# Kernel tuning notes

Measured on AMD Instinct MI355X. Metric: run time of the kernel, lower is better.

## Reference

```python
import jax, jax.numpy as jnp
import numpy as np

EPS = 1e-5


def setup_inputs() -> dict:
    key = jax.random.key(0)
    ks = jax.random.split(key, 8)
    g, p, d, h, w = 32, 64, 512, 24, 8
    hw = h * w
    return {
        "gal_fea": jax.random.normal(ks[0], (g, d, h, w), dtype=jnp.float32),
        "prob_fea": jax.random.normal(ks[1], (p, d, h, w), dtype=jnp.float32),
        "bn_weight": jnp.ones((1,), jnp.float32),
        "bn_bias": jnp.zeros((1,), jnp.float32),
        "bn_mean": jax.random.normal(ks[2], (1,), jnp.float32) * 0.1,
        "bn_var": jax.random.uniform(ks[3], (1,), jnp.float32, 0.5, 1.5),
        "fc_weight": jax.random.normal(ks[4], (1, 2 * hw), jnp.float32) * 0.05,
        "fc_bias": jnp.zeros((1,), jnp.float32),
        "lbn_weight": jnp.ones((1,), jnp.float32),
        "lbn_bias": jnp.zeros((1,), jnp.float32),
        "lbn_mean": jax.random.normal(ks[5], (1,), jnp.float32) * 0.1,
        "lbn_var": jax.random.uniform(ks[6], (1,), jnp.float32, 0.5, 1.5),
    }


def reference(gal_fea, prob_fea, bn_weight, bn_bias, bn_mean, bn_var,
              fc_weight, fc_bias, lbn_weight, lbn_bias, lbn_mean, lbn_var):
    g, d, h, w = gal_fea.shape
    p = prob_fea.shape[0]
    hw = h * w
    # 1x1 conv with probe pixels as kernels == batched correlation (QK^T style)
    gal = gal_fea.reshape(g, d, hw)                                  # [g, d, hw_x]
    ker = jnp.transpose(prob_fea, (0, 2, 3, 1)).reshape(p, hw, d)    # [p, hw_y, d]
    s = jnp.einsum('gdx,pyd->gpyx', gal, ker)                        # [g, p, hw_y, hw_x]
    # dual-axis max pooling, then concat: [g, p, 2*hw]
    score = jnp.concatenate([s.max(axis=2), s.max(axis=3)], axis=-1)
    # BatchNorm1d(1) in eval mode: scalar affine with running stats
    score = (score - bn_mean) * (bn_weight / jnp.sqrt(bn_var + EPS)) + bn_bias
    # fc: Linear(2*hw, 1)
    score = score.reshape(g * p, 2 * hw) @ fc_weight[0] + fc_bias[0]  # [g*p]
    score = score.reshape(g, p)
    # logit BatchNorm1d(1), eval mode
    score = (score - lbn_mean) * (lbn_weight / jnp.sqrt(lbn_var + EPS)) + lbn_bias
    return jax.nn.sigmoid(score / 10.0)
```

## Files before the change

kernel.cpp:

```cpp
#include <hip/hip_runtime.h>
#include <hip/hip_bf16.h>
#include <cstdint>
#include <cstddef>

#define NG 32
#define NP 64
#define ND 512
#define HW 192
#define EPSV 1e-5f

typedef _Float16 half8 __attribute__((ext_vector_type(8)));
typedef float floatx4 __attribute__((ext_vector_type(4)));
typedef float floatx16 __attribute__((ext_vector_type(16)));

__global__ __launch_bounds__(256) void transpose_cvt_all(const float* __restrict__ gal,
                                                         const float* __restrict__ prob,
                                                         _Float16* __restrict__ galT,
                                                         _Float16* __restrict__ probT) {
  __shared__ float tile[32][33];
  const int z = blockIdx.z;
  const float* sp;
  _Float16* dp;
  if (z < NP) {
    sp = prob + (size_t)z * ND * HW;
    dp = probT + (size_t)z * HW * ND;
  } else {
    sp = gal + (size_t)(z - NP) * ND * HW;
    dp = galT + (size_t)(z - NP) * HW * ND;
  }
  const int k0 = blockIdx.x * 32;
  const int s0 = blockIdx.y * 32;
  const int tx = threadIdx.x & 31, ty = threadIdx.x >> 5;
#pragma unroll
  for (int i = ty; i < 32; i += 8)
    tile[i][tx] = sp[(size_t)(k0 + i) * HW + s0 + tx];
  __syncthreads();
#pragma unroll
  for (int i = ty; i < 32; i += 8)
    dp[(size_t)(s0 + i) * ND + k0 + tx] = (_Float16)tile[tx][i];
}

__device__ __forceinline__ void g2l16(const void* g, void* l) {
  __builtin_amdgcn_global_load_lds(
      (const __attribute__((address_space(1))) void*)g,
      (__attribute__((address_space(3))) void*)l, 16, 0, 0);
}

__global__ __launch_bounds__(256, 2) void qaconv_main(
    const _Float16* __restrict__ galT, const _Float16* __restrict__ probT,
    const float* __restrict__ bn_w, const float* __restrict__ bn_b,
    const float* __restrict__ bn_m, const float* __restrict__ bn_v,
    const float* __restrict__ fc_w, const float* __restrict__ fc_b,
    const float* __restrict__ lbn_w, const float* __restrict__ lbn_b,
    const float* __restrict__ lbn_m, const float* __restrict__ lbn_v,
    float* __restrict__ out) {
  __shared__ __align__(16) char shraw[192 * 66 * 4];
  __shared__ float colpart[2][HW];
  __shared__ float wsum[4];
  char* tileA = shraw;
  char* tileB = shraw + 24576;
  float(*rowbuf)[66] = (float(*)[66])shraw;

  const int bid = blockIdx.x;
  const int g = bid >> 6, p = bid & 63;
  const int t = threadIdx.x;
  const int lane = t & 63, wid = t >> 6;
  const int wr = wid & 1;
  const int wc = wid >> 1;
  const int l31 = lane & 31, hi = lane >> 5;

  const _Float16* pA = probT + (size_t)p * HW * ND;
  const _Float16* pB = galT + (size_t)g * HW * ND;

  floatx16 acc[3][3];
#pragma unroll
  for (int i = 0; i < 3; ++i)
#pragma unroll
    for (int j = 0; j < 3; ++j) acc[i][j] = (floatx16)0.f;

  const int srow = t >> 3;
  const int s = (t & 7) ^ (srow & 7);
  const _Float16* gA = pA + (size_t)srow * ND + s * 8;
  const _Float16* gB = pB + (size_t)srow * ND + s * 8;
  const int ldst = wid * 1024;

  for (int kt = 0; kt < 8; ++kt) {
    const int kb = kt * 64;
    __syncthreads();
#pragma unroll
    for (int r = 0; r < 6; ++r) {
      g2l16(gA + (size_t)r * 32 * ND + kb, tileA + r * 4096 + ldst);
      g2l16(gB + (size_t)r * 32 * ND + kb, tileB + r * 4096 + ldst);
    }
    __syncthreads();
#pragma unroll
    for (int kc = 0; kc < 4; ++kc) {
      half8 af[3], bf[3];
      const int sl = kc * 2 + hi;
#pragma unroll
      for (int f = 0; f < 3; ++f) {
        const int ra = wr * 96 + f * 32 + l31;
        af[f] = *(const half8*)(tileA + ra * 128 + ((sl ^ (ra & 7)) << 4));
        const int rb = wc * 96 + f * 32 + l31;
        bf[f] = *(const half8*)(tileB + rb * 128 + ((sl ^ (rb & 7)) << 4));
      }
      __builtin_amdgcn_s_setprio(1);
#pragma unroll
      for (int i = 0; i < 3; ++i)
#pragma unroll
        for (int j = 0; j < 3; ++j)
          acc[i][j] =
              __builtin_amdgcn_mfma_f32_32x32x16_f16(af[i], bf[j], acc[i][j], 0, 0, 0);
      __builtin_amdgcn_s_setprio(0);
    }
  }

  float cm[3];
#pragma unroll
  for (int fb = 0; fb < 3; ++fb) {
    float v = -3.4e38f;
#pragma unroll
    for (int fa = 0; fa < 3; ++fa)
#pragma unroll
      for (int e = 0; e < 16; ++e) v = fmaxf(v, acc[fa][fb][e]);
    v = fmaxf(v, __shfl_xor(v, 32));
    cm[fb] = v;
  }
  if (lane < 32) {
#pragma unroll
    for (int fb = 0; fb < 3; ++fb) colpart[wr][wc * 96 + fb * 32 + lane] = cm[fb];
  }

  __syncthreads();
#pragma unroll
  for (int fa = 0; fa < 3; ++fa)
#pragma unroll
    for (int e = 0; e < 16; ++e) {
      const float rv =
          fmaxf(fmaxf(acc[fa][0][e], acc[fa][1][e]), acc[fa][2][e]);
      const int Y = wr * 96 + fa * 32 + (e & 3) + 8 * (e >> 2) + 4 * hi;
      rowbuf[Y][wc * 32 + l31] = rv;
    }
  __syncthreads();

  float partial = 0.f;
  if (t < HW) {
    float rmax = -3.4e38f;
#pragma unroll
    for (int j = 0; j < 16; ++j) {
      const floatx4 v = *(const floatx4*)&rowbuf[t][j * 4];
      rmax = fmaxf(rmax, fmaxf(fmaxf(v[0], v[1]), fmaxf(v[2], v[3])));
    }
    const float cmax = fmaxf(colpart[0][t], colpart[1][t]);
    const float scale = bn_w[0] / sqrtf(bn_v[0] + EPSV);
    const float m = bn_m[0], b = bn_b[0];
    partial = ((cmax - m) * scale + b) * fc_w[t] +
              ((rmax - m) * scale + b) * fc_w[HW + t];
  }
#pragma unroll
  for (int off = 1; off < 64; off <<= 1) partial += __shfl_xor(partial, off);
  if (lane == 0) wsum[wid] = partial;
  __syncthreads();
  if (t == 0) {
    const float sum = fc_b[0] + wsum[0] + wsum[1] + wsum[2] + wsum[3];
    const float logit = (sum - lbn_m[0]) * (lbn_w[0] / sqrtf(lbn_v[0] + EPSV)) + lbn_b[0];
    out[bid] = 1.f / (1.f + expf(-logit * 0.1f));
  }
}

__global__ __launch_bounds__(256) void qaconv_naive(
    const float* __restrict__ gal, const float* __restrict__ prob,
    const float* __restrict__ bn_w, const float* __restrict__ bn_b,
    const float* __restrict__ bn_m, const float* __restrict__ bn_v,
    const float* __restrict__ fc_w, const float* __restrict__ fc_b,
    const float* __restrict__ lbn_w, const float* __restrict__ lbn_b,
    const float* __restrict__ lbn_m, const float* __restrict__ lbn_v,
    float* __restrict__ out) {
  __shared__ float prow[ND];
  __shared__ float rowmaxs[HW];
  __shared__ float colmaxs[HW];
  __shared__ float red[4];
  const int bid = blockIdx.x;
  const int g = bid >> 6, p = bid & 63;
  const int t = threadIdx.x, lane = t & 63, wid = t >> 6;
  const float* gp = gal + (size_t)g * ND * HW;
  const float* pp = prob + (size_t)p * ND * HW;
  float colmax = -3.4e38f;
  for (int y = 0; y < HW; ++y) {
    for (int k = t; k < ND; k += 256) prow[k] = pp[(size_t)k * HW + y];
    __syncthreads();
    float sv = -3.4e38f;
    if (t < HW) {
      sv = 0.f;
      for (int k = 0; k < ND; ++k) sv = fmaf(prow[k], gp[(size_t)k * HW + t], sv);
      colmax = fmaxf(colmax, sv);
    }
    float m = sv;
#pragma unroll
    for (int off = 1; off < 64; off <<= 1) m = fmaxf(m, __shfl_xor(m, off));
    if (lane == 0) red[wid] = m;
    __syncthreads();
    if (t == 0) rowmaxs[y] = fmaxf(fmaxf(red[0], red[1]), fmaxf(red[2], red[3]));
    __syncthreads();
  }
  if (t < HW) colmaxs[t] = colmax;
  __syncthreads();
  float partial = 0.f;
  for (int j = t; j < 2 * HW; j += 256) {
    const float v = (j < HW) ? colmaxs[j] : rowmaxs[j - HW];
    const float sc = (v - bn_m[0]) * (bn_w[0] / sqrtf(bn_v[0] + EPSV)) + bn_b[0];
    partial += sc * fc_w[j];
  }
#pragma unroll
  for (int off = 1; off < 64; off <<= 1) partial += __shfl_xor(partial, off);
  if (lane == 0) red[wid] = partial;
  __syncthreads();
  if (t == 0) {
    const float sum = fc_b[0] + red[0] + red[1] + red[2] + red[3];
    const float logit = (sum - lbn_m[0]) * (lbn_w[0] / sqrtf(lbn_v[0] + EPSV)) + lbn_b[0];
    out[bid] = 1.f / (1.f + expf(-logit * 0.1f));
  }
}

extern "C" void kernel_launch(void* const* d_in, const int* in_sizes, int n_in,
                              void* d_out, int out_size, void* d_ws, size_t ws_size,
                              hipStream_t stream) {
  const float* gal = (const float*)d_in[0];
  const float* prob = (const float*)d_in[1];
  const float* bn_w = (const float*)d_in[2];
  const float* bn_b = (const float*)d_in[3];
  const float* bn_m = (const float*)d_in[4];
  const float* bn_v = (const float*)d_in[5];
  const float* fc_w = (const float*)d_in[6];
  const float* fc_b = (const float*)d_in[7];
  const float* lbn_w = (const float*)d_in[8];
  const float* lbn_b = (const float*)d_in[9];
  const float* lbn_m = (const float*)d_in[10];
  const float* lbn_v = (const float*)d_in[11];
  float* out = (float*)d_out;

  const size_t ws_needed = (size_t)(NP + NG) * HW * ND * sizeof(_Float16);
  if (ws_size >= ws_needed) {
    _Float16* probT = (_Float16*)d_ws;
    _Float16* galT = probT + (size_t)NP * HW * ND;
    transpose_cvt_all<<<dim3(16, 6, NP + NG), dim3(256), 0, stream>>>(gal, prob, galT, probT);
    qaconv_main<<<dim3(NG * NP), dim3(256), 0, stream>>>(
        galT, probT, bn_w, bn_b, bn_m, bn_v, fc_w, fc_b, lbn_w, lbn_b, lbn_m, lbn_v, out);
  } else {
    qaconv_naive<<<dim3(NG * NP), dim3(256), 0, stream>>>(
        gal, prob, bn_w, bn_b, bn_m, bn_v, fc_w, fc_b, lbn_w, lbn_b, lbn_m, lbn_v, out);
  }
}
```

Before: 99.10 us.

## Process two probes per block with register-fed A operands and double-buffered gallery tiles

The main kernel now computes two probe images per block against one gallery image, so each staged gallery tile in LDS is reused across both probes. Probe data is pre-packed into an MFMA-fragment layout and loaded straight into registers, software-pipelined one k-chunk ahead. Gallery tiles are double-buffered in LDS so the next stage loads while the current one computes. The cost is a larger accumulator set (18 tiles instead of 9), higher register pressure and likely lower occupancy, plus an extra prep kernel launch.

```diff
diff --git a/kernel.cpp b/kernel.cpp
--- a/kernel.cpp
+++ b/kernel.cpp
@@ -13,23 +13,24 @@
 typedef float floatx4 __attribute__((ext_vector_type(4)));
 typedef float floatx16 __attribute__((ext_vector_type(16)));
 
-__global__ __launch_bounds__(256) void transpose_cvt_all(const float* __restrict__ gal,
-                                                         const float* __restrict__ prob,
-                                                         _Float16* __restrict__ galT,
-                                                         _Float16* __restrict__ probT) {
+__global__ __launch_bounds__(192) void prep_probe(const float* __restrict__ prob,
+                                                  _Float16* __restrict__ probT2) {
+  const int p = blockIdx.x, s = blockIdx.y;
+  const int r = threadIdx.x;
+  const float* src = prob + ((size_t)p * ND + s * 8) * HW + r;
+  half8 h;
+#pragma unroll
+  for (int j = 0; j < 8; ++j) h[j] = (_Float16)src[(size_t)j * HW];
+  *(half8*)(probT2 + (((size_t)p * 64 + s) * HW + r) * 8) = h;
+}
+
+__global__ __launch_bounds__(256) void prep_gal(const float* __restrict__ gal,
+                                                _Float16* __restrict__ galT) {
   __shared__ float tile[32][33];
-  const int z = blockIdx.z;
-  const float* sp;
-  _Float16* dp;
-  if (z < NP) {
-    sp = prob + (size_t)z * ND * HW;
-    dp = probT + (size_t)z * HW * ND;
-  } else {
-    sp = gal + (size_t)(z - NP) * ND * HW;
-    dp = galT + (size_t)(z - NP) * HW * ND;
-  }
-  const int k0 = blockIdx.x * 32;
-  const int s0 = blockIdx.y * 32;
+  const int zg = blockIdx.z;
+  const float* sp = gal + (size_t)zg * ND * HW;
+  _Float16* dp = galT + (size_t)zg * HW * ND;
+  const int k0 = blockIdx.x * 32, s0 = blockIdx.y * 32;
   const int tx = threadIdx.x & 31, ty = threadIdx.x >> 5;
 #pragma unroll
   for (int i = ty; i < 32; i += 8)
@@ -46,126 +47,140 @@
       (__attribute__((address_space(3))) void*)l, 16, 0, 0);
 }
 
-__global__ __launch_bounds__(256, 2) void qaconv_main(
-    const _Float16* __restrict__ galT, const _Float16* __restrict__ probT,
+__global__ __launch_bounds__(256) void qaconv_main(
+    const _Float16* __restrict__ galT, const _Float16* __restrict__ probT2,
     const float* __restrict__ bn_w, const float* __restrict__ bn_b,
     const float* __restrict__ bn_m, const float* __restrict__ bn_v,
     const float* __restrict__ fc_w, const float* __restrict__ fc_b,
     const float* __restrict__ lbn_w, const float* __restrict__ lbn_b,
     const float* __restrict__ lbn_m, const float* __restrict__ lbn_v,
     float* __restrict__ out) {
-  __shared__ __align__(16) char shraw[192 * 66 * 4];
-  __shared__ float colpart[2][HW];
-  __shared__ float wsum[4];
-  char* tileA = shraw;
-  char* tileB = shraw + 24576;
-  float(*rowbuf)[66] = (float(*)[66])shraw;
+  __shared__ __align__(16) char shmem[53824];
+  char* bufB = shmem;
+  float* rowbuf = (float*)shmem;
+  float* colp = (float*)(shmem + 50688);
+  float* wsum = (float*)(shmem + 53760);
 
   const int bid = blockIdx.x;
-  const int g = bid >> 6, p = bid & 63;
+  const int g = bid >> 5, pb = bid & 31;
   const int t = threadIdx.x;
   const int lane = t & 63, wid = t >> 6;
-  const int wr = wid & 1;
-  const int wc = wid >> 1;
+  const int q = wid >> 1, wr = wid & 1;
   const int l31 = lane & 31, hi = lane >> 5;
 
-  const _Float16* pA = probT + (size_t)p * HW * ND;
-  const _Float16* pB = galT + (size_t)g * HW * ND;
-
-  floatx16 acc[3][3];
+  const _Float16* pAq = probT2 + ((size_t)(pb * 2 + q) * 64 * HW) * 8;
+  const int arow0 = wr * 96 + l31;
+
+  const int srow = t >> 3;
+  const int sswz = (t & 7) ^ (srow & 7);
+  const _Float16* gBl = galT + (size_t)g * HW * ND + (size_t)srow * ND + sswz * 8;
+
+  floatx16 acc[3][6];
 #pragma unroll
   for (int i = 0; i < 3; ++i)
 #pragma unroll
-    for (int j = 0; j < 3; ++j) acc[i][j] = (floatx16)0.f;
-
-  const int srow = t >> 3;
-  const int s = (t & 7) ^ (srow & 7);
-  const _Float16* gA = pA + (size_t)srow * ND + s * 8;
-  const _Float16* gB = pB + (size_t)srow * ND + s * 8;
-  const int ldst = wid * 1024;
+    for (int j = 0; j < 6; ++j) acc[i][j] = (floatx16)0.f;
+
+#define STAGE_B(kt_, buf_)                                          \
+  {                                                                 \
+    char* db_ = bufB + (buf_)*24576 + wid * 1024;                   \
+    const _Float16* sb_ = gBl + (size_t)(kt_)*64;                   \
+    _Pragma("unroll") for (int r6 = 0; r6 < 6; ++r6)                \
+        g2l16(sb_ + (size_t)r6 * 32 * ND, db_ + r6 * 4096);         \
+  }
+
+#define LOAD_AF(dst, kt_, kc_)                                                   \
+  {                                                                              \
+    const _Float16* ap_ = pAq + ((size_t)((kt_)*8 + (kc_)*2 + hi) * HW) * 8;     \
+    dst[0] = *(const half8*)(ap_ + (size_t)arow0 * 8);                           \
+    dst[1] = *(const half8*)(ap_ + (size_t)(arow0 + 32) * 8);                    \
+    dst[2] = *(const half8*)(ap_ + (size_t)(arow0 + 64) * 8);                    \
+  }
+
+#define KC_BODY(kc_, AFU, AFL, nkt_, nkc_)                                       \
+  {                                                                              \
+    LOAD_AF(AFL, nkt_, nkc_);                                                    \
+    half8 bf[6];                                                                 \
+    const int sl_ = (kc_)*2 + hi;                                                \
+    _Pragma("unroll") for (int f = 0; f < 6; ++f) {                              \
+      const int rb_ = f * 32 + l31;                                              \
+      bf[f] = *(const half8*)(bcur + rb_ * 128 + ((sl_ ^ (rb_ & 7)) << 4));      \
+    }                                                                            \
+    __builtin_amdgcn_s_setprio(1);                                               \
+    _Pragma("unroll") for (int i = 0; i < 3; ++i)                                \
+        _Pragma("unroll") for (int j = 0; j < 6; ++j)                            \
+            acc[i][j] = __builtin_amdgcn_mfma_f32_32x32x16_f16(AFU[i], bf[j],    \
+                                                               acc[i][j], 0, 0, 0); \
+    __builtin_amdgcn_s_setprio(0);                                               \
+  }
+
+  half8 af0[3], af1[3];
+  STAGE_B(0, 0);
+  LOAD_AF(af0, 0, 0);
+  __syncthreads();
 
   for (int kt = 0; kt < 8; ++kt) {
-    const int kb = kt * 64;
-    __syncthreads();
-#pragma unroll
-    for (int r = 0; r < 6; ++r) {
-      g2l16(gA + (size_t)r * 32 * ND + kb, tileA + r * 4096 + ldst);
-      g2l16(gB + (size_t)r * 32 * ND + kb, tileB + r * 4096 + ldst);
-    }
-    __syncthreads();
-#pragma unroll
-    for (int kc = 0; kc < 4; ++kc) {
-      half8 af[3], bf[3];
-      const int sl = kc * 2 + hi;
-#pragma unroll
-      for (int f = 0; f < 3; ++f) {
-        const int ra = wr * 96 + f * 32 + l31;
-        af[f] = *(const half8*)(tileA + ra * 128 + ((sl ^ (ra & 7)) << 4));
-        const int rb = wc * 96 + f * 32 + l31;
-        bf[f] = *(const half8*)(tileB + rb * 128 + ((sl ^ (rb & 7)) << 4));
-      }
-      __builtin_amdgcn_s_setprio(1);
-#pragma unroll
-      for (int i = 0; i < 3; ++i)
-#pragma unroll
-        for (int j = 0; j < 3; ++j)
-          acc[i][j] =
-              __builtin_amdgcn_mfma_f32_32x32x16_f16(af[i], bf[j], acc[i][j], 0, 0, 0);
-      __builtin_amdgcn_s_setprio(0);
-    }
-  }
-
-  float cm[3];
-#pragma unroll
-  for (int fb = 0; fb < 3; ++fb) {
+    if (kt < 7) STAGE_B(kt + 1, (kt & 1) ^ 1);
+    const char* bcur = bufB + (kt & 1) * 24576;
+    const int nb = (kt < 7) ? kt + 1 : 7;
+    KC_BODY(0, af0, af1, kt, 1)
+    KC_BODY(1, af1, af0, kt, 2)
+    KC_BODY(2, af0, af1, kt, 3)
+    KC_BODY(3, af1, af0, nb, 0)
+    __syncthreads();
+  }
+
+#pragma unroll
+  for (int fb = 0; fb < 6; ++fb) {
     float v = -3.4e38f;
 #pragma unroll
     for (int fa = 0; fa < 3; ++fa)
 #pragma unroll
       for (int e = 0; e < 16; ++e) v = fmaxf(v, acc[fa][fb][e]);
     v = fmaxf(v, __shfl_xor(v, 32));
-    cm[fb] = v;
-  }
-  if (lane < 32) {
-#pragma unroll
-    for (int fb = 0; fb < 3; ++fb) colpart[wr][wc * 96 + fb * 32 + lane] = cm[fb];
-  }
-
-  __syncthreads();
+    if (lane < 32) colp[(q * 2 + wr) * HW + fb * 32 + lane] = v;
+  }
 #pragma unroll
   for (int fa = 0; fa < 3; ++fa)
 #pragma unroll
     for (int e = 0; e < 16; ++e) {
-      const float rv =
-          fmaxf(fmaxf(acc[fa][0][e], acc[fa][1][e]), acc[fa][2][e]);
+      float rv = acc[fa][0][e];
+#pragma unroll
+      for (int fb = 1; fb < 6; ++fb) rv = fmaxf(rv, acc[fa][fb][e]);
       const int Y = wr * 96 + fa * 32 + (e & 3) + 8 * (e >> 2) + 4 * hi;
-      rowbuf[Y][wc * 32 + l31] = rv;
+      rowbuf[((size_t)q * HW + Y) * 33 + l31] = rv;
     }
   __syncthreads();
 
-  float partial = 0.f;
-  if (t < HW) {
-    float rmax = -3.4e38f;
-#pragma unroll
-    for (int j = 0; j < 16; ++j) {
-      const floatx4 v = *(const floatx4*)&rowbuf[t][j * 4];
-      rmax = fmaxf(rmax, fmaxf(fmaxf(v[0], v[1]), fmaxf(v[2], v[3])));
+  const float scale = bn_w[0] / sqrtf(bn_v[0] + EPSV);
+  const float bm = bn_m[0], bb = bn_b[0];
+#pragma unroll
+  for (int qq = 0; qq < 2; ++qq) {
+    float partial = 0.f;
+    if (t < HW) {
+      const float* rb = rowbuf + ((size_t)qq * HW + t) * 33;
+      float rmax = rb[0];
+#pragma unroll
+      for (int j = 1; j < 32; ++j) rmax = fmaxf(rmax, rb[j]);
+      const float cmax = fmaxf(colp[(qq * 2 + 0) * HW + t], colp[(qq * 2 + 1) * HW + t]);
+      partial = ((cmax - bm) * scale + bb) * fc_w[t] +
+                ((rmax - bm) * scale + bb) * fc_w[HW + t];
     }
-    const float cmax = fmaxf(colpart[0][t], colpart[1][t]);
-    const float scale = bn_w[0] / sqrtf(bn_v[0] + EPSV);
-    const float m = bn_m[0], b = bn_b[0];
-    partial = ((cmax - m) * scale + b) * fc_w[t] +
-              ((rmax - m) * scale + b) * fc_w[HW + t];
-  }
-#pragma unroll
-  for (int off = 1; off < 64; off <<= 1) partial += __shfl_xor(partial, off);
-  if (lane == 0) wsum[wid] = partial;
-  __syncthreads();
-  if (t == 0) {
-    const float sum = fc_b[0] + wsum[0] + wsum[1] + wsum[2] + wsum[3];
+#pragma unroll
+    for (int off = 1; off < 64; off <<= 1) partial += __shfl_xor(partial, off);
+    if (lane == 0) wsum[qq * 4 + wid] = partial;
+  }
+  __syncthreads();
+  if (t < 2) {
+    const int qq = t;
+    const float sum = fc_b[0] + wsum[qq * 4 + 0] + wsum[qq * 4 + 1] + wsum[qq * 4 + 2] +
+                      wsum[qq * 4 + 3];
     const float logit = (sum - lbn_m[0]) * (lbn_w[0] / sqrtf(lbn_v[0] + EPSV)) + lbn_b[0];
-    out[bid] = 1.f / (1.f + expf(-logit * 0.1f));
-  }
+    out[g * NP + pb * 2 + qq] = 1.f / (1.f + expf(-logit * 0.1f));
+  }
+#undef STAGE_B
+#undef LOAD_AF
+#undef KC_BODY
 }
 
 __global__ __launch_bounds__(256) void qaconv_naive(
@@ -239,13 +254,16 @@
   const float* lbn_v = (const float*)d_in[11];
   float* out = (float*)d_out;
 
-  const size_t ws_needed = (size_t)(NP + NG) * HW * ND * sizeof(_Float16);
+  const size_t probT2_elems = (size_t)NP * 64 * HW * 8;
+  const size_t galT_elems = (size_t)NG * HW * ND;
+  const size_t ws_needed = (probT2_elems + galT_elems) * sizeof(_Float16);
   if (ws_size >= ws_needed) {
-    _Float16* probT = (_Float16*)d_ws;
-    _Float16* galT = probT + (size_t)NP * HW * ND;
-    transpose_cvt_all<<<dim3(16, 6, NP + NG), dim3(256), 0, stream>>>(gal, prob, galT, probT);
-    qaconv_main<<<dim3(NG * NP), dim3(256), 0, stream>>>(
-        galT, probT, bn_w, bn_b, bn_m, bn_v, fc_w, fc_b, lbn_w, lbn_b, lbn_m, lbn_v, out);
+    _Float16* probT2 = (_Float16*)d_ws;
+    _Float16* galT = probT2 + probT2_elems;
+    prep_probe<<<dim3(NP, 64), dim3(192), 0, stream>>>(prob, probT2);
+    prep_gal<<<dim3(16, 6, NG), dim3(256), 0, stream>>>(gal, galT);
+    qaconv_main<<<dim3(NG * 32), dim3(256), 0, stream>>>(
+        galT, probT2, bn_w, bn_b, bn_m, bn_v, fc_w, fc_b, lbn_w, lbn_b, lbn_m, lbn_v, out);
   } else {
     qaconv_naive<<<dim3(NG * NP), dim3(256), 0, stream>>>(
         gal, prob, bn_w, bn_b, bn_m, bn_v, fc_w, fc_b, lbn_w, lbn_b, lbn_m, lbn_v, out);
```

Result: slower. 125.0 us (+26.1%).
